# Performance work log

Measured on AMD Instinct MI355X. Metric: run time of the kernel, lower is better.

Reference implementation:

```python
import jax, jax.numpy as jnp
import numpy as np

NUM_LAYERS = 2
D = 1024
DIN = 2048
N_STATE = 16
K = 4
EPS = 1e-5


def layer_norm(x, w, b):
    m = jnp.mean(x, axis=-1, keepdims=True)
    v = jnp.mean(jnp.square(x - m), axis=-1, keepdims=True)
    return (x - m) * jax.lax.rsqrt(v + EPS) * w + b


def selective_ssm(x, A_log, Wdt, b_dt, WB, WC, D_skip):
    # x: [B, L, DIN]; diagonal selective SSM (Mamba-style)
    A = -jnp.exp(A_log)                      # [DIN, N]
    dt = jax.nn.softplus(x @ Wdt + b_dt)     # [B, L, DIN]
    Bm = x @ WB                              # [B, L, N]
    Cm = x @ WC                              # [B, L, N]

    def step(h, inp):
        x_t, dt_t, B_t, C_t = inp            # [B,DIN],[B,DIN],[B,N],[B,N]
        dA = jnp.exp(dt_t[..., None] * A)    # [B, DIN, N]
        h = h * dA + (dt_t * x_t)[..., None] * B_t[:, None, :]
        y = jnp.einsum('bdn,bn->bd', h, C_t)
        return h, y

    xs = (x.transpose(1, 0, 2), dt.transpose(1, 0, 2),
          Bm.transpose(1, 0, 2), Cm.transpose(1, 0, 2))
    h0 = jnp.zeros((x.shape[0], x.shape[2], N_STATE), x.dtype)
    h_last, ys = jax.lax.scan(step, h0, xs)
    y = ys.transpose(1, 0, 2) + x * D_skip
    return y, h_last


def causal_dwconv(x, w, b):
    # x: [B, L, DIN]; w: [K, DIN] depthwise causal conv
    xp = jnp.pad(x, ((0, 0), (K - 1, 0), (0, 0)))
    out = jax.lax.conv_general_dilated(
        xp, w[:, None, :], (1,), 'VALID',
        dimension_numbers=('NWC', 'WIO', 'NWC'),
        feature_group_count=x.shape[-1])
    return out + b


def setup_inputs() -> dict:
    key = jax.random.key(0)
    ks = jax.random.split(key, 12)
    s = 0.02
    B, L = 2, 2048
    return {
        'x': jax.random.normal(ks[0], (B, L, D), jnp.float32),
        'pos_emb': jax.random.normal(ks[1], (L, D), jnp.float32) * s,
        'norm_w': jnp.ones((NUM_LAYERS, D), jnp.float32),
        'norm_b': jnp.zeros((NUM_LAYERS, D), jnp.float32),
        'Win': jax.random.normal(ks[2], (NUM_LAYERS, D, DIN), jnp.float32) * s,
        'b_in': jnp.zeros((NUM_LAYERS, DIN), jnp.float32),
        'A_log': jax.random.uniform(ks[3], (NUM_LAYERS, DIN, N_STATE), jnp.float32),
        'Wdt': jax.random.normal(ks[4], (NUM_LAYERS, DIN, DIN), jnp.float32) * s,
        'b_dt': jax.random.normal(ks[5], (NUM_LAYERS, DIN), jnp.float32) - 4.0,
        'WB': jax.random.normal(ks[6], (NUM_LAYERS, DIN, N_STATE), jnp.float32) * s,
        'WC': jax.random.normal(ks[7], (NUM_LAYERS, DIN, N_STATE), jnp.float32) * s,
        'D_skip': jnp.ones((NUM_LAYERS, DIN), jnp.float32),
        'conv_w': jax.random.normal(ks[8], (NUM_LAYERS, K, DIN), jnp.float32) * s,
        'conv_b': jnp.zeros((NUM_LAYERS, DIN), jnp.float32),
        'Wout': jax.random.normal(ks[9], (NUM_LAYERS, DIN, D), jnp.float32) * s,
        'b_out': jnp.zeros((NUM_LAYERS, D), jnp.float32),
        'fnorm_w': jnp.ones((D,), jnp.float32),
        'fnorm_b': jnp.zeros((D,), jnp.float32),
    }


def reference(x, pos_emb, norm_w, norm_b, Win, b_in, A_log, Wdt, b_dt, WB, WC,
              D_skip, conv_w, conv_b, Wout, b_out, fnorm_w, fnorm_b):
    L = x.shape[1]
    x = x + pos_emb[:L]
    for i in range(NUM_LAYERS):
        res = x
        h = layer_norm(x, norm_w[i], norm_b[i])
        h = h @ Win[i] + b_in[i]                       # [B, L, DIN]
        y_ssm, _ = selective_ssm(h, A_log[i], Wdt[i], b_dt[i], WB[i], WC[i], D_skip[i])
        y_conv = jax.nn.silu(causal_dwconv(h, conv_w[i], conv_b[i]))
        g = y_ssm * jax.nn.sigmoid(y_conv)             # gating
        x = g @ Wout[i] + b_out[i] + res               # dropout is identity (eval)
    return layer_norm(x, fnorm_w, fnorm_b)
```

## Files before the change

### kernel.cpp

```cpp
#include <hip/hip_runtime.h>
#include <cstdint>
#include <cstddef>

#define D_MODEL 1024
#define DIN     2048
#define NSTATE  16
#define LSEQ    2048
#define NBATCH  2
#define NROWS   (NBATCH*LSEQ)
#define NCOL    (DIN + 128)
#define CCH     64
#define TC      (LSEQ/CCH)
#define LOG2E   1.4426950408889634f

typedef float  f32x4  __attribute__((ext_vector_type(4)));
typedef short  bf16x8 __attribute__((ext_vector_type(8)));
typedef unsigned short us8 __attribute__((ext_vector_type(8)));

__device__ __forceinline__ unsigned short f2bf(float f) {
  union { float f; unsigned u; } c; c.f = f;
  unsigned x = c.u + 0x7fffu + ((c.u >> 16) & 1u);
  return (unsigned short)(x >> 16);
}
__device__ __forceinline__ float bf2f(unsigned short u) {
  union { unsigned u; float f; } c; c.u = (unsigned)u << 16; return c.f;
}
__device__ __forceinline__ float sigmoidf_(float x) {
  return __builtin_amdgcn_rcpf(1.f + __expf(-x));
}
__device__ __forceinline__ float softplusf_(float x) {
  return fmaxf(x, 0.f) + __logf(1.f + __expf(-fabsf(x)));
}

__device__ __forceinline__ void gll16(const void* g, void* l) {
  __builtin_amdgcn_global_load_lds(
      (const __attribute__((address_space(1))) void*)g,
      (__attribute__((address_space(3))) void*)l, 16, 0, 0);
}

__global__ __launch_bounds__(256) void ln_kernel(const float* __restrict__ Xin,
    const float* __restrict__ pos, const unsigned short* __restrict__ P, int nP,
    const float* __restrict__ bex, const float* __restrict__ w,
    const float* __restrict__ b, unsigned short* __restrict__ outB,
    float* __restrict__ outF, float* __restrict__ Xw) {
  const int row = blockIdx.x, t = threadIdx.x;
  float4 v = *(const float4*)(Xin + (size_t)row * D_MODEL + t * 4);
  if (pos) {
    const float4 p = *(const float4*)(pos + (size_t)(row & (LSEQ - 1)) * D_MODEL + t * 4);
    v.x += p.x; v.y += p.y; v.z += p.z; v.w += p.w;
  }
  if (P) {
    const size_t MN = (size_t)NROWS * D_MODEL;
    const size_t e = (size_t)row * D_MODEL + t * 4;
    float a0 = 0.f, a1 = 0.f, a2 = 0.f, a3 = 0.f;
#pragma unroll 4
    for (int k = 0; k < nP; k++) {
      const ushort4 u = *(const ushort4*)(P + k * MN + e);
      a0 += bf2f(u.x); a1 += bf2f(u.y); a2 += bf2f(u.z); a3 += bf2f(u.w);
    }
    const float4 be = *(const float4*)(bex + t * 4);
    v.x += a0 + be.x; v.y += a1 + be.y; v.z += a2 + be.z; v.w += a3 + be.w;
  }
  if (Xw) *(float4*)(Xw + (size_t)row * D_MODEL + t * 4) = v;
  float s  = v.x + v.y + v.z + v.w;
  float s2 = v.x * v.x + v.y * v.y + v.z * v.z + v.w * v.w;
#pragma unroll
  for (int o = 1; o < 64; o <<= 1) { s += __shfl_xor(s, o, 64); s2 += __shfl_xor(s2, o, 64); }
  __shared__ float ps[8];
  int wv = t >> 6;
  if ((t & 63) == 0) { ps[wv] = s; ps[wv + 4] = s2; }
  __syncthreads();
  s  = ps[0] + ps[1] + ps[2] + ps[3];
  s2 = ps[4] + ps[5] + ps[6] + ps[7];
  float mean = s * (1.f / D_MODEL);
  float var  = s2 * (1.f / D_MODEL) - mean * mean;
  float rs   = rsqrtf(var + 1e-5f);
  const float4 wv4 = *(const float4*)(w + t * 4);
  const float4 bv4 = *(const float4*)(b + t * 4);
  float o0 = (v.x - mean) * rs * wv4.x + bv4.x;
  float o1 = (v.y - mean) * rs * wv4.y + bv4.y;
  float o2 = (v.z - mean) * rs * wv4.z + bv4.z;
  float o3 = (v.w - mean) * rs * wv4.w + bv4.w;
  if (outB) {
    ushort4 o; o.x = f2bf(o0); o.y = f2bf(o1); o.z = f2bf(o2); o.w = f2bf(o3);
    *(ushort4*)(outB + (size_t)row * D_MODEL + t * 4) = o;
  } else {
    float4 o; o.x = o0; o.y = o1; o.z = o2; o.w = o3;
    *(float4*)(outF + (size_t)row * D_MODEL + t * 4) = o;
  }
}

__global__ __launch_bounds__(256) void tcvt_kernel(const float* __restrict__ in,
    unsigned short* __restrict__ out, int K_, int N_) {
  __shared__ float tile[64][68];
  int n0 = blockIdx.x * 64, k0 = blockIdx.y * 64;
  int t = threadIdx.x;
  int r = t >> 4, cc = (t & 15) * 4;
#pragma unroll
  for (int j = 0; j < 4; j++) {
    const float4 v = *(const float4*)(in + (size_t)(k0 + r + j * 16) * N_ + n0 + cc);
    tile[r + j * 16][cc + 0] = v.x; tile[r + j * 16][cc + 1] = v.y;
    tile[r + j * 16][cc + 2] = v.z; tile[r + j * 16][cc + 3] = v.w;
  }
  __syncthreads();
  int nr = t >> 2, kc = (t & 3) * 16;
  unsigned u[8];
#pragma unroll
  for (int i = 0; i < 8; i++) {
    unsigned lo = f2bf(tile[kc + 2 * i][nr]);
    unsigned hi = f2bf(tile[kc + 2 * i + 1][nr]);
    u[i] = lo | (hi << 16);
  }
  uint4* dst = (uint4*)(out + (size_t)(n0 + nr) * K_ + k0 + kc);
  uint4 w0; w0.x = u[0]; w0.y = u[1]; w0.z = u[2]; w0.w = u[3];
  uint4 w1; w1.x = u[4]; w1.y = u[5]; w1.z = u[6]; w1.w = u[7];
  dst[0] = w0; dst[1] = w1;
}

__global__ __launch_bounds__(256) void wprep_kernel(const float* __restrict__ WB,
    const float* __restrict__ WC, const float* __restrict__ b_dt,
    unsigned short* __restrict__ Wt, float* __restrict__ bias2) {
  int id = blockIdx.x * 256 + threadIdx.x;
  if (id < 65536) {
    int k = id & (DIN - 1);
    int n2 = id >> 11;
    float v = (n2 < NSTATE) ? WB[(size_t)k * NSTATE + n2]
                            : WC[(size_t)k * NSTATE + (n2 - NSTATE)];
    Wt[(size_t)(DIN + n2) * DIN + k] = f2bf(v);
  } else if (id < 90112) {
    int z = id - 65536;
    uint4 zz; zz.x = zz.y = zz.z = zz.w = 0u;
    *(uint4*)(Wt + (size_t)2080 * DIN + (size_t)z * 8) = zz;
  } else if (id < 90112 + NCOL) {
    int i = id - 90112;
    bias2[i] = (i < DIN) ? b_dt[i] : 0.f;
  }
}

__global__ __launch_bounds__(256) void gemm_kernel(
    const unsigned short* __restrict__ A, const unsigned short* __restrict__ Bt,
    const float* __restrict__ bias, unsigned short* __restrict__ outP,
    int M, int N, int Kfull, int kLen) {
  __shared__ unsigned short sA[2][128 * 32];
  __shared__ unsigned short sB[2][128 * 32];
  const int t = threadIdx.x;
  const int lane = t & 63, wave = t >> 6;
  const int wr = wave >> 1, wc = wave & 1;

  const int gx = gridDim.x, gy = gridDim.y;
  const int orig = (blockIdx.z * gy + blockIdx.y) * gx + blockIdx.x;
  const int nwg = gx * gy * gridDim.z;
  const int q = nwg >> 3, r = nwg & 7;
  const int xcd = orig & 7, pp = orig >> 3;
  const int wgid = (xcd < r) ? (xcd * (q + 1) + pp)
                             : (r * (q + 1) + (xcd - r) * q + pp);
  const int nt = wgid % gx;
  const int mt = (wgid / gx) % gy;
  const int ks = wgid / (gx * gy);
  const int m0 = mt * 128, n0 = nt * 128;

  const int ar = t >> 2, ac = (t & 3) * 8;
  const int wseg = wave * 16 * 32;
  const int lr = lane & 15, lk = (lane >> 4) * 8;

  f32x4 acc[4][4];
#pragma unroll
  for (int m = 0; m < 4; m++)
#pragma unroll
    for (int n = 0; n < 4; n++) acc[m][n] = (f32x4)0.f;

  const int kBeg = ks * kLen;
  const int NT = kLen >> 5;

  auto STAGE = [&](int bi, int k0) {
    gll16(A  + (size_t)(m0 + ar) * Kfull + k0 + ac,      &sA[bi][wseg]);
    gll16(A  + (size_t)(m0 + 64 + ar) * Kfull + k0 + ac, &sA[bi][64 * 32 + wseg]);
    gll16(Bt + (size_t)(n0 + ar) * Kfull + k0 + ac,      &sB[bi][wseg]);
    gll16(Bt + (size_t)(n0 + 64 + ar) * Kfull + k0 + ac, &sB[bi][64 * 32 + wseg]);
  };

  STAGE(0, kBeg);
  __syncthreads();
  for (int tt = 0; tt < NT; ++tt) {
    const int bi = tt & 1;
    if (tt + 1 < NT) STAGE(bi ^ 1, kBeg + ((tt + 1) << 5));
    bf16x8 af[4], bg[4];
#pragma unroll
    for (int m = 0; m < 4; m++)
      af[m] = *(const bf16x8*)(&sA[bi][(wr * 64 + m * 16 + lr) * 32 + lk]);
#pragma unroll
    for (int n = 0; n < 4; n++)
      bg[n] = *(const bf16x8*)(&sB[bi][(wc * 64 + n * 16 + lr) * 32 + lk]);
#pragma unroll
    for (int m = 0; m < 4; m++)
#pragma unroll
      for (int n = 0; n < 4; n++)
        acc[m][n] = __builtin_amdgcn_mfma_f32_16x16x32_bf16(af[m], bg[n], acc[m][n], 0, 0, 0);
    __syncthreads();
  }

  unsigned short* out = outP + (size_t)ks * M * N;
  const int lq = lane >> 4;
#pragma unroll
  for (int m = 0; m < 4; m++) {
    int row = m0 + wr * 64 + m * 16 + lq * 4;
#pragma unroll
    for (int n = 0; n < 4; n++) {
      int col = n0 + wc * 64 + n * 16 + lr;
      float bv = (bias && ks == 0) ? bias[col] : 0.f;
#pragma unroll
      for (int j = 0; j < 4; j++)
        out[(size_t)(row + j) * N + col] = f2bf(acc[m][n][j] + bv);
    }
  }
}

__global__ __launch_bounds__(256) void hfin_kernel(const unsigned short* __restrict__ P,
    const float* __restrict__ bias, unsigned short* __restrict__ Hbf) {
  const size_t e = ((size_t)blockIdx.x * 256 + threadIdx.x) * 4;
  const int col = (int)(e & (DIN - 1));
  const ushort4 u0 = *(const ushort4*)(P + e);
  const ushort4 u1 = *(const ushort4*)(P + (size_t)NROWS * DIN + e);
  const float4 b = *(const float4*)(bias + col);
  ushort4 o;
  o.x = f2bf(bf2f(u0.x) + bf2f(u1.x) + b.x);
  o.y = f2bf(bf2f(u0.y) + bf2f(u1.y) + b.y);
  o.z = f2bf(bf2f(u0.z) + bf2f(u1.z) + b.z);
  o.w = f2bf(bf2f(u0.w) + bf2f(u1.w) + b.w);
  *(ushort4*)(Hbf + e) = o;
}

__global__ __launch_bounds__(256) void scan1_kernel(
    const unsigned short* __restrict__ DTP, const unsigned short* __restrict__ Hbf,
    const float* __restrict__ A_log, float* __restrict__ Hc, float* __restrict__ Pc) {
  const unsigned short* DT1 = DTP + (size_t)NROWS * NCOL;
  const int tid = threadIdx.x;
  const int d0 = blockIdx.x * 256, d = d0 + tid;
  const int b = blockIdx.y, c = blockIdx.z;
  __shared__ unsigned short ssp[TC][256];
  __shared__ unsigned short sxx[TC][256];
  __shared__ float sBC[TC][32];
  const size_t base = (size_t)b * LSEQ + c * TC;
#pragma unroll
  for (int it = 0; it < TC * 32 / 256; ++it) {
    int idx = it * 256 + tid;
    int tt = idx >> 5, cc = (idx & 31) * 8;
    us8 a = *(const us8*)(DTP + (base + tt) * NCOL + d0 + cc);
    us8 bb = *(const us8*)(DT1 + (base + tt) * NCOL + d0 + cc);
    us8 o;
#pragma unroll
    for (int j = 0; j < 8; j++) o[j] = f2bf(softplusf_(bf2f(a[j]) + bf2f(bb[j])));
    *(us8*)&ssp[tt][cc] = o;
    *(us8*)&sxx[tt][cc] = *(const us8*)(Hbf + (base + tt) * DIN + d0 + cc);
  }
  if (tid < TC * 4) {
    int tt = tid >> 2, cc = (tid & 3) * 8;
    us8 v0 = *(const us8*)(DTP + (base + tt) * NCOL + DIN + cc);
    us8 v1 = *(const us8*)(DT1 + (base + tt) * NCOL + DIN + cc);
#pragma unroll
    for (int j = 0; j < 8; j++) sBC[tt][cc + j] = bf2f(v0[j]) + bf2f(v1[j]);
  }
  float a2[16], h[16];
#pragma unroll
  for (int n = 0; n < 16; n++) {
    a2[n] = -__expf(A_log[(size_t)d * NSTATE + n]);
    h[n] = 0.f;
  }
  __syncthreads();
  float S = 0.f;
  for (int tt = 0; tt < TC; ++tt) {
    float sp = bf2f(ssp[tt][tid]);
    float x  = bf2f(sxx[tt][tid]);
    S += sp;
    float sx = sp * x;
#pragma unroll
    for (int n = 0; n < 16; n++)
      h[n] = fmaf(h[n], __expf(sp * a2[n]), sx * sBC[tt][n]);
  }
  const size_t chain = ((size_t)c * (NBATCH * DIN) + (size_t)b * DIN + d) * 16;
#pragma unroll
  for (int n = 0; n < 16; n++) {
    Hc[chain + n] = h[n];
    Pc[chain + n] = __expf(S * a2[n]);
  }
}

__global__ __launch_bounds__(256) void scomb_kernel(float* __restrict__ Hc,
    const float* __restrict__ Pc) {
  const size_t id = (size_t)blockIdx.x * 256 + threadIdx.x;
  const size_t stride = (size_t)NBATCH * DIN * NSTATE;
  float h = 0.f;
  for (int c = 0; c < CCH; c++) {
    size_t o = (size_t)c * stride + id;
    float hl = Hc[o], p = Pc[o];
    Hc[o] = h;
    h = fmaf(p, h, hl);
  }
}

__global__ __launch_bounds__(256) void scan2g_kernel(
    const unsigned short* __restrict__ DTP, const unsigned short* __restrict__ Hbf,
    const float* __restrict__ A_log, const float* __restrict__ Hinit,
    const float* __restrict__ cw, const float* __restrict__ cb,
    const float* __restrict__ dsk, unsigned short* __restrict__ G) {
  const unsigned short* DT1 = DTP + (size_t)NROWS * NCOL;
  const int tid = threadIdx.x;
  const int d0 = blockIdx.x * 256, d = d0 + tid;
  const int b = blockIdx.y, c = blockIdx.z;
  __shared__ unsigned short ssp[TC][256];
  __shared__ unsigned short sxx[TC][256];
  __shared__ float sBC[TC][32];
  const size_t base = (size_t)b * LSEQ + c * TC;
#pragma unroll
  for (int it = 0; it < TC * 32 / 256; ++it) {
    int idx = it * 256 + tid;
    int tt = idx >> 5, cc = (idx & 31) * 8;
    us8 a = *(const us8*)(DTP + (base + tt) * NCOL + d0 + cc);
    us8 bb = *(const us8*)(DT1 + (base + tt) * NCOL + d0 + cc);
    us8 o;
#pragma unroll
    for (int j = 0; j < 8; j++) o[j] = f2bf(softplusf_(bf2f(a[j]) + bf2f(bb[j])));
    *(us8*)&ssp[tt][cc] = o;
    *(us8*)&sxx[tt][cc] = *(const us8*)(Hbf + (base + tt) * DIN + d0 + cc);
  }
  if (tid < TC * 4) {
    int tt = tid >> 2, cc = (tid & 3) * 8;
    us8 v0 = *(const us8*)(DTP + (base + tt) * NCOL + DIN + cc);
    us8 v1 = *(const us8*)(DT1 + (base + tt) * NCOL + DIN + cc);
#pragma unroll
    for (int j = 0; j < 8; j++) sBC[tt][cc + j] = bf2f(v0[j]) + bf2f(v1[j]);
  }
  const size_t chain = ((size_t)c * (NBATCH * DIN) + (size_t)b * DIN + d) * 16;
  float a2[16], h[16];
#pragma unroll
  for (int n = 0; n < 16; n++) {
    a2[n] = -__expf(A_log[(size_t)d * NSTATE + n]);
    h[n] = Hinit[chain + n];
  }
  const float w0 = cw[d], w1 = cw[DIN + d], w2 = cw[2 * DIN + d], w3 = cw[3 * DIN + d];
  const float cbv = cb[d], dsv = dsk[d];
  const int t0 = c * TC;
  float xm1 = (t0 >= 1) ? bf2f(Hbf[(base - 1) * DIN + d]) : 0.f;
  float xm2 = (t0 >= 2) ? bf2f(Hbf[(base - 2) * DIN + d]) : 0.f;
  float xm3 = (t0 >= 3) ? bf2f(Hbf[(base - 3) * DIN + d]) : 0.f;
  __syncthreads();
  for (int tt = 0; tt < TC; ++tt) {
    float sp = bf2f(ssp[tt][tid]);
    float x  = bf2f(sxx[tt][tid]);
    float sx = sp * x;
    float y0 = 0.f, y1 = 0.f, y2 = 0.f, y3 = 0.f;
#pragma unroll
    for (int n = 0; n < 16; n += 4) {
      h[n]     = fmaf(h[n],     __expf(sp * a2[n]),     sx * sBC[tt][n]);
      h[n + 1] = fmaf(h[n + 1], __expf(sp * a2[n + 1]), sx * sBC[tt][n + 1]);
      h[n + 2] = fmaf(h[n + 2], __expf(sp * a2[n + 2]), sx * sBC[tt][n + 2]);
      h[n + 3] = fmaf(h[n + 3], __expf(sp * a2[n + 3]), sx * sBC[tt][n + 3]);
      y0 = fmaf(h[n],     sBC[tt][16 + n],     y0);
      y1 = fmaf(h[n + 1], sBC[tt][16 + n + 1], y1);
      y2 = fmaf(h[n + 2], sBC[tt][16 + n + 2], y2);
      y3 = fmaf(h[n + 3], sBC[tt][16 + n + 3], y3);
    }
    float y = (y0 + y1) + (y2 + y3);
    float a = cbv + w0 * xm3 + w1 * xm2 + w2 * xm1 + w3 * x;
    float sl = a * sigmoidf_(a);
    float g = (y + x * dsv) * sigmoidf_(sl);
    G[(base + tt) * DIN + d] = f2bf(g);
    xm3 = xm2; xm2 = xm1; xm1 = x;
  }
}

extern "C" void kernel_launch(void* const* d_in, const int* in_sizes, int n_in,
                              void* d_out, int out_size, void* d_ws, size_t ws_size,
                              hipStream_t stream) {
  const float* x_in   = (const float*)d_in[0];
  const float* pos    = (const float*)d_in[1];
  const float* norm_w = (const float*)d_in[2];
  const float* norm_b = (const float*)d_in[3];
  const float* Win    = (const float*)d_in[4];
  const float* b_in   = (const float*)d_in[5];
  const float* A_log  = (const float*)d_in[6];
  const float* Wdt    = (const float*)d_in[7];
  const float* b_dt   = (const float*)d_in[8];
  const float* WB     = (const float*)d_in[9];
  const float* WC     = (const float*)d_in[10];
  const float* Dsk    = (const float*)d_in[11];
  const float* conv_w = (const float*)d_in[12];
  const float* conv_b = (const float*)d_in[13];
  const float* Wout   = (const float*)d_in[14];
  const float* b_out  = (const float*)d_in[15];
  const float* fnw    = (const float*)d_in[16];
  const float* fnb    = (const float*)d_in[17];

  uint8_t* ws = (uint8_t*)d_ws;
  constexpr size_t OFF_X     = 0;
  constexpr size_t OFF_HBF   = 16777216;
  constexpr size_t OFF_DT    = 33554432;
  constexpr size_t OFF_XG    = 69206016;
  constexpr size_t OFF_HC    = 85983232;
  constexpr size_t OFF_PC    = 102760448;
  constexpr size_t OFF_WINT  = 119537664;
  constexpr size_t OFF_WDT   = 123731968;
  constexpr size_t OFF_WOUT  = 132644864;
  constexpr size_t OFF_BIAS2 = 136839168;
  constexpr size_t WS_NEEDED = 136847872;
  if (ws_size < WS_NEEDED) return;

  float* X             = (float*)(ws + OFF_X);
  unsigned short* Hbf  = (unsigned short*)(ws + OFF_HBF);
  unsigned short* DTP  = (unsigned short*)(ws + OFF_DT);
  unsigned short* Xn   = (unsigned short*)(ws + OFF_XG);
  unsigned short* Gb   = (unsigned short*)(ws + OFF_XG);
  float* Hc            = (float*)(ws + OFF_HC);
  float* Pc            = (float*)(ws + OFF_PC);
  unsigned short* WinT   = (unsigned short*)(ws + OFF_WINT);
  unsigned short* WdtBCT = (unsigned short*)(ws + OFF_WDT);
  unsigned short* WoutT  = (unsigned short*)(ws + OFF_WOUT);
  float* bias2         = (float*)(ws + OFF_BIAS2);

  for (int i = 0; i < 2; i++) {
    tcvt_kernel<<<dim3(2048 / 64, 1024 / 64), 256, 0, stream>>>(
        Win + (size_t)i * D_MODEL * DIN, WinT, 1024, 2048);
    tcvt_kernel<<<dim3(2048 / 64, 2048 / 64), 256, 0, stream>>>(
        Wdt + (size_t)i * DIN * DIN, WdtBCT, 2048, 2048);
    wprep_kernel<<<361, 256, 0, stream>>>(
        WB + (size_t)i * DIN * NSTATE, WC + (size_t)i * DIN * NSTATE,
        b_dt + (size_t)i * DIN, WdtBCT, bias2);
    tcvt_kernel<<<dim3(1024 / 64, 2048 / 64), 256, 0, stream>>>(
        Wout + (size_t)i * DIN * D_MODEL, WoutT, 2048, 1024);

    if (i == 0)
      ln_kernel<<<4096, 256, 0, stream>>>(x_in, pos, nullptr, 0, nullptr,
                                          norm_w, norm_b, Xn, nullptr, X);
    else
      ln_kernel<<<4096, 256, 0, stream>>>(X, nullptr, DTP, 4, b_out,
                                          norm_w + D_MODEL, norm_b + D_MODEL,
                                          Xn, nullptr, X);
    gemm_kernel<<<dim3(16, 32, 2), 256, 0, stream>>>(
        Xn, WinT, nullptr, DTP, NROWS, DIN, D_MODEL, 512);
    hfin_kernel<<<8192, 256, 0, stream>>>(DTP, b_in + (size_t)i * DIN, Hbf);
    gemm_kernel<<<dim3(17, 32, 2), 256, 0, stream>>>(
        Hbf, WdtBCT, bias2, DTP, NROWS, NCOL, DIN, 1024);
    scan1_kernel<<<dim3(DIN / 256, NBATCH, CCH), 256, 0, stream>>>(
        DTP, Hbf, A_log + (size_t)i * DIN * NSTATE, Hc, Pc);
    scomb_kernel<<<(NBATCH * DIN * NSTATE) / 256, 256, 0, stream>>>(Hc, Pc);
    scan2g_kernel<<<dim3(DIN / 256, NBATCH, CCH), 256, 0, stream>>>(
        DTP, Hbf, A_log + (size_t)i * DIN * NSTATE, Hc,
        conv_w + (size_t)i * 4 * DIN, conv_b + (size_t)i * DIN,
        Dsk + (size_t)i * DIN, Gb);
    gemm_kernel<<<dim3(8, 32, 4), 256, 0, stream>>>(
        Gb, WoutT, nullptr, DTP, NROWS, D_MODEL, DIN, 512);
  }

  ln_kernel<<<4096, 256, 0, stream>>>(X, nullptr, DTP, 4, b_out + D_MODEL,
                                      fnw, fnb, nullptr, (float*)d_out, nullptr);
}
```

Before: 512.3 us.

## Triple-buffer GEMM LDS with XOR swizzle and batch weight prep across layers

The GEMM main loop moves from a double-buffered LDS pipeline to three stages with explicit vmcnt waits and one barrier per iteration, so global loads can run further ahead of the MFMA work. The k-chunk column assigned to each loader thread is XOR-swizzled by row, and the fragment reads use the matching swizzle, to reduce LDS bank conflicts. Weight transpose and convert kernels for both layers are now launched once before the layer loop as batched grids, which cuts the number of launches and lets each launch fill more of the GPU. The cost is more workspace and more LDS per block, which may reduce occupancy.

Measured after the change: 502.6 us. Within noise of the previous version (-1.9%).

```diff
diff --git a/kernel.cpp b/kernel.cpp
--- a/kernel.cpp
+++ b/kernel.cpp
@@ -11,7 +11,6 @@
 #define NCOL    (DIN + 128)
 #define CCH     64
 #define TC      (LSEQ/CCH)
-#define LOG2E   1.4426950408889634f
 
 typedef float  f32x4  __attribute__((ext_vector_type(4)));
 typedef short  bf16x8 __attribute__((ext_vector_type(8)));
@@ -90,8 +89,11 @@
   }
 }
 
-__global__ __launch_bounds__(256) void tcvt_kernel(const float* __restrict__ in,
-    unsigned short* __restrict__ out, int K_, int N_) {
+__global__ __launch_bounds__(256) void tcvt_kernel(const float* __restrict__ in0,
+    unsigned short* __restrict__ out0, int K_, int N_,
+    size_t inLS, size_t outLS) {
+  const float* in = in0 + (size_t)blockIdx.z * inLS;
+  unsigned short* out = out0 + (size_t)blockIdx.z * outLS;
   __shared__ float tile[64][68];
   int n0 = blockIdx.x * 64, k0 = blockIdx.y * 64;
   int t = threadIdx.x;
@@ -117,9 +119,15 @@
   dst[0] = w0; dst[1] = w1;
 }
 
-__global__ __launch_bounds__(256) void wprep_kernel(const float* __restrict__ WB,
-    const float* __restrict__ WC, const float* __restrict__ b_dt,
-    unsigned short* __restrict__ Wt, float* __restrict__ bias2) {
+__global__ __launch_bounds__(256) void wprep_kernel(const float* __restrict__ WB0,
+    const float* __restrict__ WC0, const float* __restrict__ b_dt0,
+    unsigned short* __restrict__ Wt0, float* __restrict__ bias20) {
+  const int L = blockIdx.y;
+  const float* WB = WB0 + (size_t)L * DIN * NSTATE;
+  const float* WC = WC0 + (size_t)L * DIN * NSTATE;
+  const float* b_dt = b_dt0 + (size_t)L * DIN;
+  unsigned short* Wt = Wt0 + (size_t)L * NCOL * DIN;
+  float* bias2 = bias20 + (size_t)L * NCOL;
   int id = blockIdx.x * 256 + threadIdx.x;
   if (id < 65536) {
     int k = id & (DIN - 1);
@@ -141,8 +149,8 @@
     const unsigned short* __restrict__ A, const unsigned short* __restrict__ Bt,
     const float* __restrict__ bias, unsigned short* __restrict__ outP,
     int M, int N, int Kfull, int kLen) {
-  __shared__ unsigned short sA[2][128 * 32];
-  __shared__ unsigned short sB[2][128 * 32];
+  __shared__ unsigned short sA[3][128 * 32];
+  __shared__ unsigned short sB[3][128 * 32];
   const int t = threadIdx.x;
   const int lane = t & 63, wave = t >> 6;
   const int wr = wave >> 1, wc = wave & 1;
@@ -159,9 +167,11 @@
   const int ks = wgid / (gx * gy);
   const int m0 = mt * 128, n0 = nt * 128;
 
-  const int ar = t >> 2, ac = (t & 3) * 8;
+  const int ar = t >> 2;
+  const int acs = (((t & 3) ^ (ar & 3)) << 3);
   const int wseg = wave * 16 * 32;
-  const int lr = lane & 15, lk = (lane >> 4) * 8;
+  const int lr = lane & 15;
+  const int swA = (((lane >> 4) ^ (lr & 3)) << 3);
 
   f32x4 acc[4][4];
 #pragma unroll
@@ -173,31 +183,36 @@
   const int NT = kLen >> 5;
 
   auto STAGE = [&](int bi, int k0) {
-    gll16(A  + (size_t)(m0 + ar) * Kfull + k0 + ac,      &sA[bi][wseg]);
-    gll16(A  + (size_t)(m0 + 64 + ar) * Kfull + k0 + ac, &sA[bi][64 * 32 + wseg]);
-    gll16(Bt + (size_t)(n0 + ar) * Kfull + k0 + ac,      &sB[bi][wseg]);
-    gll16(Bt + (size_t)(n0 + 64 + ar) * Kfull + k0 + ac, &sB[bi][64 * 32 + wseg]);
+    gll16(A  + (size_t)(m0 + ar) * Kfull + k0 + acs,      &sA[bi][wseg]);
+    gll16(A  + (size_t)(m0 + 64 + ar) * Kfull + k0 + acs, &sA[bi][64 * 32 + wseg]);
+    gll16(Bt + (size_t)(n0 + ar) * Kfull + k0 + acs,      &sB[bi][wseg]);
+    gll16(Bt + (size_t)(n0 + 64 + ar) * Kfull + k0 + acs, &sB[bi][64 * 32 + wseg]);
   };
-
-  STAGE(0, kBeg);
-  __syncthreads();
-  for (int tt = 0; tt < NT; ++tt) {
-    const int bi = tt & 1;
-    if (tt + 1 < NT) STAGE(bi ^ 1, kBeg + ((tt + 1) << 5));
+  auto COMPUTE = [&](int bi) {
     bf16x8 af[4], bg[4];
 #pragma unroll
     for (int m = 0; m < 4; m++)
-      af[m] = *(const bf16x8*)(&sA[bi][(wr * 64 + m * 16 + lr) * 32 + lk]);
+      af[m] = *(const bf16x8*)(&sA[bi][(wr * 64 + m * 16 + lr) * 32 + swA]);
 #pragma unroll
     for (int n = 0; n < 4; n++)
-      bg[n] = *(const bf16x8*)(&sB[bi][(wc * 64 + n * 16 + lr) * 32 + lk]);
+      bg[n] = *(const bf16x8*)(&sB[bi][(wc * 64 + n * 16 + lr) * 32 + swA]);
 #pragma unroll
     for (int m = 0; m < 4; m++)
 #pragma unroll
       for (int n = 0; n < 4; n++)
         acc[m][n] = __builtin_amdgcn_mfma_f32_16x16x32_bf16(af[m], bg[n], acc[m][n], 0, 0, 0);
-    __syncthreads();
-  }
+  };
+
+  STAGE(0, kBeg); STAGE(1, kBeg + 32);
+  for (int tt = 0; tt < NT - 1; ++tt) {
+    asm volatile("s_waitcnt vmcnt(4)" ::: "memory");
+    __builtin_amdgcn_s_barrier();
+    if (tt + 2 < NT) STAGE((tt + 2) % 3, kBeg + ((tt + 2) << 5));
+    COMPUTE(tt % 3);
+  }
+  asm volatile("s_waitcnt vmcnt(0)" ::: "memory");
+  __builtin_amdgcn_s_barrier();
+  COMPUTE((NT - 1) % 3);
 
   unsigned short* out = outP + (size_t)ks * M * N;
   const int lq = lane >> 4;
@@ -399,10 +414,10 @@
   constexpr size_t OFF_HC    = 85983232;
   constexpr size_t OFF_PC    = 102760448;
   constexpr size_t OFF_WINT  = 119537664;
-  constexpr size_t OFF_WDT   = 123731968;
-  constexpr size_t OFF_WOUT  = 132644864;
-  constexpr size_t OFF_BIAS2 = 136839168;
-  constexpr size_t WS_NEEDED = 136847872;
+  constexpr size_t OFF_WDT   = 127926272;
+  constexpr size_t OFF_WOUT  = 145752064;
+  constexpr size_t OFF_BIAS2 = 154140672;
+  constexpr size_t WS_NEEDED = 154158080;
   if (ws_size < WS_NEEDED) return;
 
   float* X             = (float*)(ws + OFF_X);
@@ -417,16 +432,19 @@
   unsigned short* WoutT  = (unsigned short*)(ws + OFF_WOUT);
   float* bias2         = (float*)(ws + OFF_BIAS2);
 
+  tcvt_kernel<<<dim3(32, 16, 2), 256, 0, stream>>>(
+      Win, WinT, 1024, 2048, (size_t)D_MODEL * DIN, (size_t)DIN * D_MODEL);
+  tcvt_kernel<<<dim3(32, 32, 2), 256, 0, stream>>>(
+      Wdt, WdtBCT, 2048, 2048, (size_t)DIN * DIN, (size_t)NCOL * DIN);
+  tcvt_kernel<<<dim3(16, 32, 2), 256, 0, stream>>>(
+      Wout, WoutT, 2048, 1024, (size_t)DIN * D_MODEL, (size_t)D_MODEL * DIN);
+  wprep_kernel<<<dim3(361, 2), 256, 0, stream>>>(WB, WC, b_dt, WdtBCT, bias2);
+
   for (int i = 0; i < 2; i++) {
-    tcvt_kernel<<<dim3(2048 / 64, 1024 / 64), 256, 0, stream>>>(
-        Win + (size_t)i * D_MODEL * DIN, WinT, 1024, 2048);
-    tcvt_kernel<<<dim3(2048 / 64, 2048 / 64), 256, 0, stream>>>(
-        Wdt + (size_t)i * DIN * DIN, WdtBCT, 2048, 2048);
-    wprep_kernel<<<361, 256, 0, stream>>>(
-        WB + (size_t)i * DIN * NSTATE, WC + (size_t)i * DIN * NSTATE,
-        b_dt + (size_t)i * DIN, WdtBCT, bias2);
-    tcvt_kernel<<<dim3(1024 / 64, 2048 / 64), 256, 0, stream>>>(
-        Wout + (size_t)i * DIN * D_MODEL, WoutT, 2048, 1024);
+    unsigned short* WinT_i   = WinT + (size_t)i * DIN * D_MODEL;
+    unsigned short* WdtBCT_i = WdtBCT + (size_t)i * NCOL * DIN;
+    unsigned short* WoutT_i  = WoutT + (size_t)i * D_MODEL * DIN;
+    float* bias2_i           = bias2 + (size_t)i * NCOL;
 
     if (i == 0)
       ln_kernel<<<4096, 256, 0, stream>>>(x_in, pos, nullptr, 0, nullptr,
@@ -436,10 +454,10 @@
                                           norm_w + D_MODEL, norm_b + D_MODEL,
                                           Xn, nullptr, X);
     gemm_kernel<<<dim3(16, 32, 2), 256, 0, stream>>>(
-        Xn, WinT, nullptr, DTP, NROWS, DIN, D_MODEL, 512);
+        Xn, WinT_i, nullptr, DTP, NROWS, DIN, D_MODEL, 512);
     hfin_kernel<<<8192, 256, 0, stream>>>(DTP, b_in + (size_t)i * DIN, Hbf);
     gemm_kernel<<<dim3(17, 32, 2), 256, 0, stream>>>(
-        Hbf, WdtBCT, bias2, DTP, NROWS, NCOL, DIN, 1024);
+        Hbf, WdtBCT_i, bias2_i, DTP, NROWS, NCOL, DIN, 1024);
     scan1_kernel<<<dim3(DIN / 256, NBATCH, CCH), 256, 0, stream>>>(
         DTP, Hbf, A_log + (size_t)i * DIN * NSTATE, Hc, Pc);
     scomb_kernel<<<(NBATCH * DIN * NSTATE) / 256, 256, 0, stream>>>(Hc, Pc);
@@ -448,7 +466,7 @@
         conv_w + (size_t)i * 4 * DIN, conv_b + (size_t)i * DIN,
         Dsk + (size_t)i * DIN, Gb);
     gemm_kernel<<<dim3(8, 32, 4), 256, 0, stream>>>(
-        Gb, WoutT, nullptr, DTP, NROWS, D_MODEL, DIN, 512);
+        Gb, WoutT_i, nullptr, DTP, NROWS, D_MODEL, DIN, 512);
   }
 
   ln_kernel<<<4096, 256, 0, stream>>>(X, nullptr, DTP, 4, b_out + D_MODEL,
```
